# Performance work log

Hardware: AMD Instinct MI355X
Metric: run time of the kernel (lower is better)

## Reference

```python
import jax, jax.numpy as jnp
import numpy as np

EPS = 1e-5
GROUPS = 32
N_HEADS = 8
HEAD_DIM = 64


def setup_inputs() -> dict:
    key = jax.random.key(0)
    ks = jax.random.split(key, 8)
    b, c, d, w, hs = 2, 512, 16, 16, 16
    ctx_len, ctx_dim = 1024, 768
    inner = N_HEADS * HEAD_DIM  # 512
    return {
        "x": jax.random.normal(ks[0], (b, c, d, w, hs), jnp.float32),
        "context": jax.random.normal(ks[1], (b, ctx_len, ctx_dim), jnp.float32),
        "gamma": jnp.ones((c,), jnp.float32),
        "beta": jnp.zeros((c,), jnp.float32),
        "Wq": jax.random.normal(ks[2], (c, inner), jnp.float32) * (c ** -0.5),
        "Wk": jax.random.normal(ks[3], (ctx_dim, inner), jnp.float32) * (ctx_dim ** -0.5),
        "Wv": jax.random.normal(ks[4], (ctx_dim, inner), jnp.float32) * (ctx_dim ** -0.5),
        "Wo": jax.random.normal(ks[5], (inner, c), jnp.float32) * (inner ** -0.5),
        "bo": jnp.zeros((c,), jnp.float32),
    }


def reference(x, context, gamma, beta, Wq, Wk, Wv, Wo, bo):
    b, c, d, w, hs = x.shape
    n = d * w * hs  # sequence length of voxel tokens
    scale = HEAD_DIM ** -0.5

    # GroupNorm over (channels-in-group, spatial)
    xg = x.reshape(b, GROUPS, -1)
    mu = jnp.mean(xg, axis=-1, keepdims=True)
    var = jnp.mean(jnp.square(xg - mu), axis=-1, keepdims=True)
    xn = (xg - mu) * jax.lax.rsqrt(var + EPS)
    xn = xn.reshape(b, c, n) * gamma[None, :, None] + beta[None, :, None]

    x_seq = jnp.swapaxes(x.reshape(b, c, n), 1, 2)   # [b, n, c] residual
    xn_seq = jnp.swapaxes(xn, 1, 2)                   # [b, n, c]

    q = (xn_seq @ Wq).reshape(b, n, N_HEADS, HEAD_DIM)
    k = (context @ Wk).reshape(b, -1, N_HEADS, HEAD_DIM)
    v = (context @ Wv).reshape(b, -1, N_HEADS, HEAD_DIM)

    attn = jax.nn.softmax(jnp.einsum('bqhd,bkhd->bhqk', q, k) * scale, axis=-1)
    out = jnp.einsum('bhqk,bkhd->bqhd', attn, v).reshape(b, n, N_HEADS * HEAD_DIM)

    out = out @ Wo + bo  # dropout is identity in eval mode
    out = out + x_seq
    return jnp.swapaxes(out, 1, 2).reshape(b, c, d, w, hs)
```

## Files before the change

### kernel.cpp

```cpp
#include <hip/hip_runtime.h>
#include <hip/hip_bf16.h>

#define B 2
#define C 512
#define NTOK 4096
#define GROUPS 32
#define CPG 16
#define CTX 1024
#define CDIM 768
#define NH 8
#define HD 64
#define INNER 512
#define EPS 1e-5f
#define KVBLK 64
#define NCH (CTX / KVBLK)
#define LOG2E 1.44269504f

typedef unsigned short bf16_t;
typedef __attribute__((ext_vector_type(8))) short bf16x8;
typedef __attribute__((ext_vector_type(4))) float f32x4;

__device__ __forceinline__ bf16_t f2b(float f) {
    unsigned u = __float_as_uint(f);
    u += 0x7fffu + ((u >> 16) & 1u);
    return (bf16_t)(u >> 16);
}

__device__ __forceinline__ float4 pack8(const float* v) {
    union { ushort s[8]; float4 f; } u;
    #pragma unroll
    for (int j = 0; j < 8; ++j) u.s[j] = f2b(v[j]);
    return u.f;
}

__device__ __forceinline__ unsigned cvtpk(float lo, float hi) {
    unsigned r;
    asm("v_cvt_pk_bf16_f32 %0, %1, %2" : "=v"(r) : "v"(lo), "v"(hi));
    return r;
}

__device__ __forceinline__ int swz(int row, int col) {
    return row * 64 + (col ^ ((row & 7) << 3));
}

__global__ __launch_bounds__(256) void gn_partial_kernel(const float* __restrict__ x,
                                                         float2* __restrict__ partials) {
    int blk = blockIdx.x;
    const float* base = x + (size_t)blk * 4096;
    float s = 0.f, ss = 0.f;
    #pragma unroll
    for (int i = 0; i < 4; ++i) {
        float4 v = *(const float4*)&base[(threadIdx.x + i * 256) * 4];
        s += v.x + v.y + v.z + v.w;
        ss += v.x * v.x + v.y * v.y + v.z * v.z + v.w * v.w;
    }
    #pragma unroll
    for (int o = 32; o > 0; o >>= 1) { s += __shfl_xor(s, o); ss += __shfl_xor(ss, o); }
    __shared__ float ls[2][4];
    int wv = threadIdx.x >> 6, ln = threadIdx.x & 63;
    if (ln == 0) { ls[0][wv] = s; ls[1][wv] = ss; }
    __syncthreads();
    if (threadIdx.x == 0) {
        partials[blk] = make_float2(ls[0][0] + ls[0][1] + ls[0][2] + ls[0][3],
                                    ls[1][0] + ls[1][1] + ls[1][2] + ls[1][3]);
    }
}

__global__ __launch_bounds__(256) void gn_apply_kernel(const float* __restrict__ x,
                                                       const float2* __restrict__ partials,
                                                       const float* __restrict__ gamma,
                                                       const float* __restrict__ beta,
                                                       bf16_t* __restrict__ xn) {
    __shared__ float tile[32][33];
    __shared__ float gmu[2], grs[2];
    int b = blockIdx.z;
    int c0 = blockIdx.y * 32;
    int t0 = blockIdx.x * 32;
    int tid = threadIdx.x;
    if (tid < 32) {
        int gi = tid >> 4, pi = tid & 15;
        float2 pp = partials[b * C + c0 + gi * 16 + pi];
        float s = pp.x, ss = pp.y;
        #pragma unroll
        for (int o = 8; o > 0; o >>= 1) { s += __shfl_xor(s, o); ss += __shfl_xor(ss, o); }
        if (pi == 0) {
            float mu = s / (float)(CPG * NTOK);
            float var = ss / (float)(CPG * NTOK) - mu * mu;
            gmu[gi] = mu;
            grs[gi] = rsqrtf(var + EPS);
        }
    }
    int tt = tid & 31, cr = tid >> 5;
    __syncthreads();
    #pragma unroll
    for (int i = 0; i < 4; ++i) {
        int co = cr + 8 * i;
        int c = c0 + co;
        float mu = gmu[co >> 4], rs = grs[co >> 4];
        float v = x[((size_t)(b * C + c)) * NTOK + t0 + tt];
        tile[co][tt] = (v - mu) * rs * gamma[c] + beta[c];
    }
    __syncthreads();
    #pragma unroll
    for (int i = 0; i < 4; ++i) {
        int t = t0 + cr + 8 * i;
        int c = c0 + tt;
        xn[((size_t)b * NTOK + t) * C + c] = f2b(tile[tt][cr + 8 * i]);
    }
}

__global__ __launch_bounds__(256) void wcast_all_kernel(
    const float* __restrict__ Wq, const float* __restrict__ Wk,
    const float* __restrict__ Wv, const float* __restrict__ Wo,
    bf16_t* __restrict__ Wqt, bf16_t* __restrict__ Wkvt, bf16_t* __restrict__ Wot) {
    int z = blockIdx.z;
    const float* in; bf16_t* out; int K;
    if (z == 0)      { in = Wq; out = Wqt;  K = C; }
    else if (z == 1) { in = Wk; out = Wkvt; K = CDIM; }
    else if (z == 2) { in = Wv; out = Wkvt + (size_t)INNER * CDIM; K = CDIM; }
    else             { in = Wo; out = Wot;  K = INNER; }
    int k0 = blockIdx.x * 32, n0 = blockIdx.y * 32;
    if (k0 >= K) return;
    __shared__ float t[32][33];
    int xx = threadIdx.x & 31, yy = threadIdx.x >> 5;
    #pragma unroll
    for (int i = 0; i < 4; ++i)
        t[yy + 8 * i][xx] = in[(size_t)(k0 + yy + 8 * i) * INNER + n0 + xx];
    __syncthreads();
    #pragma unroll
    for (int i = 0; i < 4; ++i)
        out[(size_t)(n0 + yy + 8 * i) * K + k0 + xx] = f2b(t[xx][yy + 8 * i]);
}

template <int AFP32>
__global__ __launch_bounds__(256) void gemm_qkv_kernel(
    const void* __restrict__ Av, const bf16_t* __restrict__ Bt,
    bf16_t* __restrict__ outK, bf16_t* __restrict__ outV,
    int K, int seqshift, float oscale, int vtrans) {
    __shared__ __align__(16) bf16_t As[64][40];
    __shared__ __align__(16) bf16_t Bs[64][40];
    const int tid = threadIdx.x;
    const int l = tid & 63, w = tid >> 6;
    const int wr = w >> 1, wc = w & 1;
    const int lg = l >> 4, lr = l & 15;
    const int m0 = blockIdx.x * 64, n0 = blockIdx.y * 64;
    const int rowS = tid >> 2, c8 = (tid & 3) * 8;
    const bf16_t* pa16 = AFP32 ? nullptr : (const bf16_t*)Av + (size_t)(m0 + rowS) * K + c8;
    const float*  pa32 = AFP32 ? (const float*)Av + (size_t)(m0 + rowS) * K + c8 : nullptr;
    const bf16_t* pb = Bt + (size_t)(n0 + rowS) * K + c8;
    f32x4 acc[2][2] = {};
    float av[8];
    float4 ra, rb;
    if (AFP32) {
        *(float4*)&av[0] = *(const float4*)pa32;
        *(float4*)&av[4] = *(const float4*)(pa32 + 4);
        ra = pack8(av);
    } else {
        ra = *(const float4*)pa16;
    }
    rb = *(const float4*)pb;
    *(float4*)&As[rowS][c8] = ra;
    *(float4*)&Bs[rowS][c8] = rb;
    for (int k0 = 0; k0 < K; k0 += 32) {
        __syncthreads();
        if (k0 + 32 < K) {
            if (AFP32) {
                *(float4*)&av[0] = *(const float4*)(pa32 + k0 + 32);
                *(float4*)&av[4] = *(const float4*)(pa32 + k0 + 36);
                ra = pack8(av);
            } else {
                ra = *(const float4*)(pa16 + k0 + 32);
            }
            rb = *(const float4*)(pb + k0 + 32);
        }
        bf16x8 af[2], bfm[2];
        af[0]  = *(bf16x8*)&As[wr * 32 + lr][lg * 8];
        af[1]  = *(bf16x8*)&As[wr * 32 + 16 + lr][lg * 8];
        bfm[0] = *(bf16x8*)&Bs[wc * 32 + lr][lg * 8];
        bfm[1] = *(bf16x8*)&Bs[wc * 32 + 16 + lr][lg * 8];
        #pragma unroll
        for (int mi = 0; mi < 2; ++mi)
            #pragma unroll
            for (int ni = 0; ni < 2; ++ni)
                acc[mi][ni] = __builtin_amdgcn_mfma_f32_16x16x32_bf16(af[mi], bfm[ni], acc[mi][ni], 0, 0, 0);
        __syncthreads();
        if (k0 + 32 < K) {
            *(float4*)&As[rowS][c8] = ra;
            *(float4*)&Bs[rowS][c8] = rb;
        }
    }
    const int seqmask = (1 << seqshift) - 1;
    #pragma unroll
    for (int ni = 0; ni < 2; ++ni) {
        int n = n0 + wc * 32 + ni * 16 + lr;
        int nn = n & (INNER - 1);
        int h = nn >> 6, dd = nn & 63;
        bool isV = (n >= INNER);
        #pragma unroll
        for (int mi = 0; mi < 2; ++mi) {
            int mb = m0 + wr * 32 + mi * 16 + lg * 4;
            int bidx = mb >> seqshift, seqb = mb & seqmask;
            if (isV && vtrans) {
                ushort4 pv;
                pv.x = f2b(acc[mi][ni][0] * oscale);
                pv.y = f2b(acc[mi][ni][1] * oscale);
                pv.z = f2b(acc[mi][ni][2] * oscale);
                pv.w = f2b(acc[mi][ni][3] * oscale);
                *(ushort4*)&outV[((size_t)(bidx * NH + h) * HD + dd) * (size_t)(seqmask + 1) + seqb] = pv;
            } else {
                bf16_t* dst = isV ? outV : outK;
                #pragma unroll
                for (int r = 0; r < 4; ++r)
                    dst[(((size_t)(bidx * NH + h) << seqshift) + seqb + r) * HD + dd] =
                        f2b(acc[mi][ni][r] * oscale);
            }
        }
    }
}

__global__ __launch_bounds__(256) void gemm_o_kernel(
    const bf16_t* __restrict__ A, const bf16_t* __restrict__ Bt,
    const float* __restrict__ bo, const float* __restrict__ x,
    float* __restrict__ out) {
    __shared__ __align__(16) bf16_t As[64][40];
    __shared__ __align__(16) bf16_t Bs[64][40];
    const int tid = threadIdx.x;
    const int l = tid & 63, w = tid >> 6;
    const int wr = w >> 1, wc = w & 1;
    const int lg = l >> 4, lr = l & 15;
    const int m0 = blockIdx.x * 64, n0 = blockIdx.y * 64;
    const int rowS = tid >> 2, c8 = (tid & 3) * 8;
    const bf16_t* pa = A  + (size_t)(m0 + rowS) * INNER + c8;
    const bf16_t* pb = Bt + (size_t)(n0 + rowS) * INNER + c8;
    f32x4 acc[2][2] = {};
    float4 ra = *(const float4*)pa;
    float4 rb = *(const float4*)pb;
    *(float4*)&As[rowS][c8] = ra;
    *(float4*)&Bs[rowS][c8] = rb;
    for (int k0 = 0; k0 < INNER; k0 += 32) {
        __syncthreads();
        if (k0 + 32 < INNER) {
            ra = *(const float4*)(pa + k0 + 32);
            rb = *(const float4*)(pb + k0 + 32);
        }
        bf16x8 af[2], bfm[2];
        af[0]  = *(bf16x8*)&As[wr * 32 + lr][lg * 8];
        af[1]  = *(bf16x8*)&As[wr * 32 + 16 + lr][lg * 8];
        bfm[0] = *(bf16x8*)&Bs[wc * 32 + lr][lg * 8];
        bfm[1] = *(bf16x8*)&Bs[wc * 32 + 16 + lr][lg * 8];
        #pragma unroll
        for (int mi = 0; mi < 2; ++mi)
            #pragma unroll
            for (int ni = 0; ni < 2; ++ni)
                acc[mi][ni] = __builtin_amdgcn_mfma_f32_16x16x32_bf16(af[mi], bfm[ni], acc[mi][ni], 0, 0, 0);
        __syncthreads();
        if (k0 + 32 < INNER) {
            *(float4*)&As[rowS][c8] = ra;
            *(float4*)&Bs[rowS][c8] = rb;
        }
    }
    #pragma unroll
    for (int mi = 0; mi < 2; ++mi) {
        int mb = m0 + wr * 32 + mi * 16 + lg * 4;
        int t = mb & (NTOK - 1);
        int bb = mb >> 12;
        #pragma unroll
        for (int ni = 0; ni < 2; ++ni) {
            int cc = n0 + wc * 32 + ni * 16 + lr;
            size_t o = (((size_t)(bb * C + cc)) << 12) + t;
            float4 xr = *(const float4*)&x[o];
            float bias = bo[cc];
            float4 ov;
            ov.x = acc[mi][ni][0] + bias + xr.x;
            ov.y = acc[mi][ni][1] + bias + xr.y;
            ov.z = acc[mi][ni][2] + bias + xr.z;
            ov.w = acc[mi][ni][3] + bias + xr.w;
            *(float4*)&out[o] = ov;
        }
    }
}

__global__ __launch_bounds__(256) void attn_kernel(
    const bf16_t* __restrict__ Q, const bf16_t* __restrict__ Kb,
    const bf16_t* __restrict__ Vt, bf16_t* __restrict__ AO) {
    __shared__ __align__(16) bf16_t Ks[64 * 64];
    __shared__ __align__(16) bf16_t Vs[64 * 64];
    __shared__ __align__(16) bf16_t Ps[4][16 * 64];
    const int tid = threadIdx.x;
    const int l = tid & 63, w = tid >> 6;
    const int lg = l >> 4, lr = l & 15;
    const int bh = blockIdx.x >> 6;
    const int tile = blockIdx.x & 63;
    const int b = bh >> 3, h = bh & 7;
    const int t0 = tile * 64 + w * 16;

    const bf16_t* qbase = Q + ((size_t)bh * NTOK + t0 + lr) * HD;
    bf16x8 qf[2];
    qf[0] = *(const bf16x8*)&qbase[lg * 8];
    qf[1] = *(const bf16x8*)&qbase[32 + lg * 8];

    f32x4 acc[4] = {};
    float mrow = -1e30f;
    float lrow = 0.f;

    const bf16_t* kbase = Kb + (size_t)bh * CTX * HD;
    const bf16_t* vbase = Vt + (size_t)bh * HD * CTX;
    const int srow = tid >> 3, sc8 = (tid & 7) * 8;

    float4 kr0 = *(const float4*)&kbase[(size_t)srow * HD + sc8];
    float4 kr1 = *(const float4*)&kbase[(size_t)(srow + 32) * HD + sc8];
    float4 vr0 = *(const float4*)&vbase[(size_t)srow * CTX + sc8];
    float4 vr1 = *(const float4*)&vbase[(size_t)(srow + 32) * CTX + sc8];
    *(float4*)&Ks[swz(srow, sc8)] = kr0;
    *(float4*)&Ks[swz(srow + 32, sc8)] = kr1;
    *(float4*)&Vs[swz(srow, sc8)] = vr0;
    *(float4*)&Vs[swz(srow + 32, sc8)] = vr1;

    for (int c = 0; c < NCH; ++c) {
        __syncthreads();
        if (c + 1 < NCH) {
            int k1 = (c + 1) * KVBLK;
            kr0 = *(const float4*)&kbase[(size_t)(k1 + srow) * HD + sc8];
            kr1 = *(const float4*)&kbase[(size_t)(k1 + srow + 32) * HD + sc8];
            vr0 = *(const float4*)&vbase[(size_t)srow * CTX + k1 + sc8];
            vr1 = *(const float4*)&vbase[(size_t)(srow + 32) * CTX + k1 + sc8];
        }
        f32x4 sf[4] = {};
        #pragma unroll
        for (int ks = 0; ks < 2; ++ks)
            #pragma unroll
            for (int ni = 0; ni < 4; ++ni) {
                bf16x8 kf = *(bf16x8*)&Ks[swz(ni * 16 + lr, ks * 32 + lg * 8)];
                sf[ni] = __builtin_amdgcn_mfma_f32_16x16x32_bf16(kf, qf[ks], sf[ni], 0, 0, 0);
            }
        float cm = sf[0][0];
        #pragma unroll
        for (int ni = 0; ni < 4; ++ni)
            #pragma unroll
            for (int r = 0; r < 4; ++r) cm = fmaxf(cm, sf[ni][r]);
        cm = fmaxf(cm, __shfl_xor(cm, 16));
        cm = fmaxf(cm, __shfl_xor(cm, 32));
        float mn = fmaxf(mrow, cm);
        float scl = __builtin_amdgcn_exp2f(mrow - mn);
        mrow = mn;
        float p[4][4];
        float rs = 0.f;
        #pragma unroll
        for (int ni = 0; ni < 4; ++ni)
            #pragma unroll
            for (int r = 0; r < 4; ++r) {
                p[ni][r] = __builtin_amdgcn_exp2f(sf[ni][r] - mn);
                rs += p[ni][r];
            }
        rs += __shfl_xor(rs, 16);
        rs += __shfl_xor(rs, 32);
        lrow = lrow * scl + rs;
        #pragma unroll
        for (int ni = 0; ni < 4; ++ni) {
            unsigned pk0 = cvtpk(p[ni][0], p[ni][1]);
            unsigned pk1 = cvtpk(p[ni][2], p[ni][3]);
            *(uint2*)&Ps[w][swz(lr, ni * 16 + 4 * lg)] = make_uint2(pk0, pk1);
        }
        float sclr[4];
        #pragma unroll
        for (int r = 0; r < 4; ++r)
            sclr[r] = __shfl(scl, (l & 48) | (4 * lg + r));
        #pragma unroll
        for (int ni = 0; ni < 4; ++ni)
            #pragma unroll
            for (int r = 0; r < 4; ++r) acc[ni][r] *= sclr[r];
        #pragma unroll
        for (int ks = 0; ks < 2; ++ks) {
            bf16x8 pf = *(bf16x8*)&Ps[w][swz(lr, ks * 32 + 8 * lg)];
            #pragma unroll
            for (int ni = 0; ni < 4; ++ni) {
                bf16x8 vf = *(bf16x8*)&Vs[swz(ni * 16 + lr, ks * 32 + lg * 8)];
                acc[ni] = __builtin_amdgcn_mfma_f32_16x16x32_bf16(pf, vf, acc[ni], 0, 0, 0);
            }
        }
        __syncthreads();
        if (c + 1 < NCH) {
            *(float4*)&Ks[swz(srow, sc8)] = kr0;
            *(float4*)&Ks[swz(srow + 32, sc8)] = kr1;
            *(float4*)&Vs[swz(srow, sc8)] = vr0;
            *(float4*)&Vs[swz(srow + 32, sc8)] = vr1;
        }
    }

    float lfin[4];
    #pragma unroll
    for (int r = 0; r < 4; ++r)
        lfin[r] = __shfl(lrow, (l & 48) | (4 * lg + r));
    #pragma unroll
    for (int ni = 0; ni < 4; ++ni)
        #pragma unroll
        for (int r = 0; r < 4; ++r) {
            int t = t0 + lg * 4 + r;
            AO[((size_t)b * NTOK + t) * INNER + h * HD + ni * 16 + lr] =
                f2b(acc[ni][r] / lfin[r]);
        }
}

extern "C" void kernel_launch(void* const* d_in, const int* in_sizes, int n_in,
                              void* d_out, int out_size, void* d_ws, size_t ws_size,
                              hipStream_t stream) {
    const float* x       = (const float*)d_in[0];
    const float* context = (const float*)d_in[1];
    const float* gamma   = (const float*)d_in[2];
    const float* beta    = (const float*)d_in[3];
    const float* Wq      = (const float*)d_in[4];
    const float* Wk      = (const float*)d_in[5];
    const float* Wv      = (const float*)d_in[6];
    const float* Wo      = (const float*)d_in[7];
    const float* bo      = (const float*)d_in[8];
    float* out = (float*)d_out;

    char* p = (char*)d_ws;
    float2* parts = (float2*)p;          p += 1024 * sizeof(float2);
    bf16_t* xn   = (bf16_t*)p;           p += (size_t)B * NTOK * C * 2;
    bf16_t* Wqt  = (bf16_t*)p;           p += (size_t)INNER * C * 2;
    bf16_t* Wkvt = (bf16_t*)p;           p += (size_t)2 * INNER * CDIM * 2;
    bf16_t* Wot  = (bf16_t*)p;           p += (size_t)C * INNER * 2;
    bf16_t* qb   = (bf16_t*)p;           p += (size_t)B * NH * NTOK * HD * 2;
    bf16_t* kb   = (bf16_t*)p;           p += (size_t)B * NH * CTX * HD * 2;
    bf16_t* vb   = (bf16_t*)p;           p += (size_t)B * NH * CTX * HD * 2;
    bf16_t* ao   = (bf16_t*)p;           p += (size_t)B * NTOK * INNER * 2;

    hipLaunchKernelGGL(gn_partial_kernel, dim3(B * C), dim3(256), 0, stream, x, parts);
    hipLaunchKernelGGL(gn_apply_kernel, dim3(NTOK / 32, C / 32, B), dim3(256), 0, stream,
                       x, parts, gamma, beta, xn);
    hipLaunchKernelGGL(wcast_all_kernel, dim3(24, 16, 4), dim3(256), 0, stream,
                       Wq, Wk, Wv, Wo, Wqt, Wkvt, Wot);
    hipLaunchKernelGGL((gemm_qkv_kernel<0>), dim3(128, 8), dim3(256), 0, stream,
                       (const void*)xn, Wqt, qb, qb, C, 12, 0.125f * LOG2E, 0);
    hipLaunchKernelGGL((gemm_qkv_kernel<1>), dim3(32, 16), dim3(256), 0, stream,
                       (const void*)context, Wkvt, kb, vb, CDIM, 10, 1.0f, 1);
    hipLaunchKernelGGL(attn_kernel, dim3(B * NH * (NTOK / 64)), dim3(256), 0, stream,
                       qb, kb, vb, ao);
    hipLaunchKernelGGL(gemm_o_kernel, dim3(128, 8), dim3(256), 0, stream,
                       ao, Wot, bo, x, out);
}
```

Before: 171.5 us.

## Merge GN stats and weight cast kernels; use 64-deep K steps in GEMMs

Fuses the GroupNorm partial-sum kernel and the weight transpose/cast kernel into a single launch, removing one kernel launch. Both GEMM kernels now stage two 32-wide K slices per iteration, halving the number of barrier pairs per K loop and issuing twice as many global loads ahead of the MFMAs, at the cost of more LDS and registers. The attention epilogue replaces per-element division with a hardware reciprocal multiply, which slightly changes rounding.

```diff
diff --git a/kernel.cpp b/kernel.cpp
--- a/kernel.cpp
+++ b/kernel.cpp
@@ -43,27 +43,51 @@
     return row * 64 + (col ^ ((row & 7) << 3));
 }
 
-__global__ __launch_bounds__(256) void gn_partial_kernel(const float* __restrict__ x,
-                                                         float2* __restrict__ partials) {
+__global__ __launch_bounds__(256) void prep_kernel(
+    const float* __restrict__ x, float2* __restrict__ partials,
+    const float* __restrict__ Wq, const float* __restrict__ Wk,
+    const float* __restrict__ Wv, const float* __restrict__ Wo,
+    bf16_t* __restrict__ Wqt, bf16_t* __restrict__ Wkvt, bf16_t* __restrict__ Wot) {
     int blk = blockIdx.x;
-    const float* base = x + (size_t)blk * 4096;
-    float s = 0.f, ss = 0.f;
-    #pragma unroll
-    for (int i = 0; i < 4; ++i) {
-        float4 v = *(const float4*)&base[(threadIdx.x + i * 256) * 4];
-        s += v.x + v.y + v.z + v.w;
-        ss += v.x * v.x + v.y * v.y + v.z * v.z + v.w * v.w;
-    }
-    #pragma unroll
-    for (int o = 32; o > 0; o >>= 1) { s += __shfl_xor(s, o); ss += __shfl_xor(ss, o); }
-    __shared__ float ls[2][4];
-    int wv = threadIdx.x >> 6, ln = threadIdx.x & 63;
-    if (ln == 0) { ls[0][wv] = s; ls[1][wv] = ss; }
+    if (blk < B * C) {
+        const float* base = x + (size_t)blk * 4096;
+        float s = 0.f, ss = 0.f;
+        #pragma unroll
+        for (int i = 0; i < 4; ++i) {
+            float4 v = *(const float4*)&base[(threadIdx.x + i * 256) * 4];
+            s += v.x + v.y + v.z + v.w;
+            ss += v.x * v.x + v.y * v.y + v.z * v.z + v.w * v.w;
+        }
+        #pragma unroll
+        for (int o = 32; o > 0; o >>= 1) { s += __shfl_xor(s, o); ss += __shfl_xor(ss, o); }
+        __shared__ float ls[2][4];
+        int wv = threadIdx.x >> 6, ln = threadIdx.x & 63;
+        if (ln == 0) { ls[0][wv] = s; ls[1][wv] = ss; }
+        __syncthreads();
+        if (threadIdx.x == 0)
+            partials[blk] = make_float2(ls[0][0] + ls[0][1] + ls[0][2] + ls[0][3],
+                                        ls[1][0] + ls[1][1] + ls[1][2] + ls[1][3]);
+        return;
+    }
+    int id = blk - B * C;
+    int z = id / 384;
+    int rem = id - z * 384;
+    int k0 = (rem % 24) * 32, n0 = (rem / 24) * 32;
+    const float* in; bf16_t* out; int K;
+    if (z == 0)      { in = Wq; out = Wqt;  K = C; }
+    else if (z == 1) { in = Wk; out = Wkvt; K = CDIM; }
+    else if (z == 2) { in = Wv; out = Wkvt + (size_t)INNER * CDIM; K = CDIM; }
+    else             { in = Wo; out = Wot;  K = INNER; }
+    if (k0 >= K) return;
+    __shared__ float t[32][33];
+    int xx = threadIdx.x & 31, yy = threadIdx.x >> 5;
+    #pragma unroll
+    for (int i = 0; i < 4; ++i)
+        t[yy + 8 * i][xx] = in[(size_t)(k0 + yy + 8 * i) * INNER + n0 + xx];
     __syncthreads();
-    if (threadIdx.x == 0) {
-        partials[blk] = make_float2(ls[0][0] + ls[0][1] + ls[0][2] + ls[0][3],
-                                    ls[1][0] + ls[1][1] + ls[1][2] + ls[1][3]);
-    }
+    #pragma unroll
+    for (int i = 0; i < 4; ++i)
+        out[(size_t)(n0 + yy + 8 * i) * K + k0 + xx] = f2b(t[xx][yy + 8 * i]);
 }
 
 __global__ __launch_bounds__(256) void gn_apply_kernel(const float* __restrict__ x,
@@ -109,36 +133,13 @@
     }
 }
 
-__global__ __launch_bounds__(256) void wcast_all_kernel(
-    const float* __restrict__ Wq, const float* __restrict__ Wk,
-    const float* __restrict__ Wv, const float* __restrict__ Wo,
-    bf16_t* __restrict__ Wqt, bf16_t* __restrict__ Wkvt, bf16_t* __restrict__ Wot) {
-    int z = blockIdx.z;
-    const float* in; bf16_t* out; int K;
-    if (z == 0)      { in = Wq; out = Wqt;  K = C; }
-    else if (z == 1) { in = Wk; out = Wkvt; K = CDIM; }
-    else if (z == 2) { in = Wv; out = Wkvt + (size_t)INNER * CDIM; K = CDIM; }
-    else             { in = Wo; out = Wot;  K = INNER; }
-    int k0 = blockIdx.x * 32, n0 = blockIdx.y * 32;
-    if (k0 >= K) return;
-    __shared__ float t[32][33];
-    int xx = threadIdx.x & 31, yy = threadIdx.x >> 5;
-    #pragma unroll
-    for (int i = 0; i < 4; ++i)
-        t[yy + 8 * i][xx] = in[(size_t)(k0 + yy + 8 * i) * INNER + n0 + xx];
-    __syncthreads();
-    #pragma unroll
-    for (int i = 0; i < 4; ++i)
-        out[(size_t)(n0 + yy + 8 * i) * K + k0 + xx] = f2b(t[xx][yy + 8 * i]);
-}
-
 template <int AFP32>
 __global__ __launch_bounds__(256) void gemm_qkv_kernel(
     const void* __restrict__ Av, const bf16_t* __restrict__ Bt,
     bf16_t* __restrict__ outK, bf16_t* __restrict__ outV,
     int K, int seqshift, float oscale, int vtrans) {
-    __shared__ __align__(16) bf16_t As[64][40];
-    __shared__ __align__(16) bf16_t Bs[64][40];
+    __shared__ __align__(16) bf16_t As[2][64][40];
+    __shared__ __align__(16) bf16_t Bs[2][64][40];
     const int tid = threadIdx.x;
     const int l = tid & 63, w = tid >> 6;
     const int wr = w >> 1, wc = w & 1;
@@ -150,45 +151,56 @@
     const bf16_t* pb = Bt + (size_t)(n0 + rowS) * K + c8;
     f32x4 acc[2][2] = {};
     float av[8];
-    float4 ra, rb;
-    if (AFP32) {
-        *(float4*)&av[0] = *(const float4*)pa32;
-        *(float4*)&av[4] = *(const float4*)(pa32 + 4);
-        ra = pack8(av);
-    } else {
-        ra = *(const float4*)pa16;
-    }
-    rb = *(const float4*)pb;
-    *(float4*)&As[rowS][c8] = ra;
-    *(float4*)&Bs[rowS][c8] = rb;
-    for (int k0 = 0; k0 < K; k0 += 32) {
-        __syncthreads();
-        if (k0 + 32 < K) {
-            if (AFP32) {
-                *(float4*)&av[0] = *(const float4*)(pa32 + k0 + 32);
-                *(float4*)&av[4] = *(const float4*)(pa32 + k0 + 36);
-                ra = pack8(av);
-            } else {
-                ra = *(const float4*)(pa16 + k0 + 32);
-            }
-            rb = *(const float4*)(pb + k0 + 32);
-        }
-        bf16x8 af[2], bfm[2];
-        af[0]  = *(bf16x8*)&As[wr * 32 + lr][lg * 8];
-        af[1]  = *(bf16x8*)&As[wr * 32 + 16 + lr][lg * 8];
-        bfm[0] = *(bf16x8*)&Bs[wc * 32 + lr][lg * 8];
-        bfm[1] = *(bf16x8*)&Bs[wc * 32 + 16 + lr][lg * 8];
-        #pragma unroll
-        for (int mi = 0; mi < 2; ++mi)
-            #pragma unroll
-            for (int ni = 0; ni < 2; ++ni)
-                acc[mi][ni] = __builtin_amdgcn_mfma_f32_16x16x32_bf16(af[mi], bfm[ni], acc[mi][ni], 0, 0, 0);
-        __syncthreads();
-        if (k0 + 32 < K) {
-            *(float4*)&As[rowS][c8] = ra;
-            *(float4*)&Bs[rowS][c8] = rb;
-        }
-    }
+    float4 ra0, ra1, rb0, rb1;
+    #define LOADA(dst, off) do { \
+        if (AFP32) { \
+            *(float4*)&av[0] = *(const float4*)(pa32 + (off)); \
+            *(float4*)&av[4] = *(const float4*)(pa32 + (off) + 4); \
+            dst = pack8(av); \
+        } else { dst = *(const float4*)(pa16 + (off)); } } while (0)
+    LOADA(ra0, 0);
+    LOADA(ra1, 32);
+    rb0 = *(const float4*)pb;
+    rb1 = *(const float4*)(pb + 32);
+    *(float4*)&As[0][rowS][c8] = ra0;
+    *(float4*)&As[1][rowS][c8] = ra1;
+    *(float4*)&Bs[0][rowS][c8] = rb0;
+    *(float4*)&Bs[1][rowS][c8] = rb1;
+    const int NIT = K >> 6;
+    for (int it = 0; it < NIT; ++it) {
+        __syncthreads();
+        if (it + 1 < NIT) {
+            int k1 = (it + 1) << 6;
+            LOADA(ra0, k1);
+            LOADA(ra1, k1 + 32);
+            rb0 = *(const float4*)(pb + k1);
+            rb1 = *(const float4*)(pb + k1 + 32);
+        }
+        bf16x8 af[2][2], bfm[2][2];
+        #pragma unroll
+        for (int ks = 0; ks < 2; ++ks) {
+            af[0][ks]  = *(bf16x8*)&As[ks][wr * 32 + lr][lg * 8];
+            af[1][ks]  = *(bf16x8*)&As[ks][wr * 32 + 16 + lr][lg * 8];
+            bfm[0][ks] = *(bf16x8*)&Bs[ks][wc * 32 + lr][lg * 8];
+            bfm[1][ks] = *(bf16x8*)&Bs[ks][wc * 32 + 16 + lr][lg * 8];
+        }
+        #pragma unroll
+        for (int ks = 0; ks < 2; ++ks)
+            #pragma unroll
+            for (int mi = 0; mi < 2; ++mi)
+                #pragma unroll
+                for (int ni = 0; ni < 2; ++ni)
+                    acc[mi][ni] = __builtin_amdgcn_mfma_f32_16x16x32_bf16(
+                        af[mi][ks], bfm[ni][ks], acc[mi][ni], 0, 0, 0);
+        __syncthreads();
+        if (it + 1 < NIT) {
+            *(float4*)&As[0][rowS][c8] = ra0;
+            *(float4*)&As[1][rowS][c8] = ra1;
+            *(float4*)&Bs[0][rowS][c8] = rb0;
+            *(float4*)&Bs[1][rowS][c8] = rb1;
+        }
+    }
+    #undef LOADA
     const int seqmask = (1 << seqshift) - 1;
     #pragma unroll
     for (int ni = 0; ni < 2; ++ni) {
@@ -222,8 +234,8 @@
     const bf16_t* __restrict__ A, const bf16_t* __restrict__ Bt,
     const float* __restrict__ bo, const float* __restrict__ x,
     float* __restrict__ out) {
-    __shared__ __align__(16) bf16_t As[64][40];
-    __shared__ __align__(16) bf16_t Bs[64][40];
+    __shared__ __align__(16) bf16_t As[2][64][40];
+    __shared__ __align__(16) bf16_t Bs[2][64][40];
     const int tid = threadIdx.x;
     const int l = tid & 63, w = tid >> 6;
     const int wr = w >> 1, wc = w & 1;
@@ -233,30 +245,46 @@
     const bf16_t* pa = A  + (size_t)(m0 + rowS) * INNER + c8;
     const bf16_t* pb = Bt + (size_t)(n0 + rowS) * INNER + c8;
     f32x4 acc[2][2] = {};
-    float4 ra = *(const float4*)pa;
-    float4 rb = *(const float4*)pb;
-    *(float4*)&As[rowS][c8] = ra;
-    *(float4*)&Bs[rowS][c8] = rb;
-    for (int k0 = 0; k0 < INNER; k0 += 32) {
-        __syncthreads();
-        if (k0 + 32 < INNER) {
-            ra = *(const float4*)(pa + k0 + 32);
-            rb = *(const float4*)(pb + k0 + 32);
-        }
-        bf16x8 af[2], bfm[2];
-        af[0]  = *(bf16x8*)&As[wr * 32 + lr][lg * 8];
-        af[1]  = *(bf16x8*)&As[wr * 32 + 16 + lr][lg * 8];
-        bfm[0] = *(bf16x8*)&Bs[wc * 32 + lr][lg * 8];
-        bfm[1] = *(bf16x8*)&Bs[wc * 32 + 16 + lr][lg * 8];
-        #pragma unroll
-        for (int mi = 0; mi < 2; ++mi)
-            #pragma unroll
-            for (int ni = 0; ni < 2; ++ni)
-                acc[mi][ni] = __builtin_amdgcn_mfma_f32_16x16x32_bf16(af[mi], bfm[ni], acc[mi][ni], 0, 0, 0);
-        __syncthreads();
-        if (k0 + 32 < INNER) {
-            *(float4*)&As[rowS][c8] = ra;
-            *(float4*)&Bs[rowS][c8] = rb;
+    float4 ra0 = *(const float4*)pa;
+    float4 ra1 = *(const float4*)(pa + 32);
+    float4 rb0 = *(const float4*)pb;
+    float4 rb1 = *(const float4*)(pb + 32);
+    *(float4*)&As[0][rowS][c8] = ra0;
+    *(float4*)&As[1][rowS][c8] = ra1;
+    *(float4*)&Bs[0][rowS][c8] = rb0;
+    *(float4*)&Bs[1][rowS][c8] = rb1;
+    const int NIT = INNER >> 6;
+    for (int it = 0; it < NIT; ++it) {
+        __syncthreads();
+        if (it + 1 < NIT) {
+            int k1 = (it + 1) << 6;
+            ra0 = *(const float4*)(pa + k1);
+            ra1 = *(const float4*)(pa + k1 + 32);
+            rb0 = *(const float4*)(pb + k1);
+            rb1 = *(const float4*)(pb + k1 + 32);
+        }
+        bf16x8 af[2][2], bfm[2][2];
+        #pragma unroll
+        for (int ks = 0; ks < 2; ++ks) {
+            af[0][ks]  = *(bf16x8*)&As[ks][wr * 32 + lr][lg * 8];
+            af[1][ks]  = *(bf16x8*)&As[ks][wr * 32 + 16 + lr][lg * 8];
+            bfm[0][ks] = *(bf16x8*)&Bs[ks][wc * 32 + lr][lg * 8];
+            bfm[1][ks] = *(bf16x8*)&Bs[ks][wc * 32 + 16 + lr][lg * 8];
+        }
+        #pragma unroll
+        for (int ks = 0; ks < 2; ++ks)
+            #pragma unroll
+            for (int mi = 0; mi < 2; ++mi)
+                #pragma unroll
+                for (int ni = 0; ni < 2; ++ni)
+                    acc[mi][ni] = __builtin_amdgcn_mfma_f32_16x16x32_bf16(
+                        af[mi][ks], bfm[ni][ks], acc[mi][ni], 0, 0, 0);
+        __syncthreads();
+        if (it + 1 < NIT) {
+            *(float4*)&As[0][rowS][c8] = ra0;
+            *(float4*)&As[1][rowS][c8] = ra1;
+            *(float4*)&Bs[0][rowS][c8] = rb0;
+            *(float4*)&Bs[1][rowS][c8] = rb1;
         }
     }
     #pragma unroll
@@ -387,17 +415,17 @@
         }
     }
 
-    float lfin[4];
+    float linv[4];
     #pragma unroll
     for (int r = 0; r < 4; ++r)
-        lfin[r] = __shfl(lrow, (l & 48) | (4 * lg + r));
+        linv[r] = __builtin_amdgcn_rcpf(__shfl(lrow, (l & 48) | (4 * lg + r)));
     #pragma unroll
     for (int ni = 0; ni < 4; ++ni)
         #pragma unroll
         for (int r = 0; r < 4; ++r) {
             int t = t0 + lg * 4 + r;
             AO[((size_t)b * NTOK + t) * INNER + h * HD + ni * 16 + lr] =
-                f2b(acc[ni][r] / lfin[r]);
+                f2b(acc[ni][r] * linv[r]);
         }
 }
 
@@ -426,11 +454,10 @@
     bf16_t* vb   = (bf16_t*)p;           p += (size_t)B * NH * CTX * HD * 2;
     bf16_t* ao   = (bf16_t*)p;           p += (size_t)B * NTOK * INNER * 2;
 
-    hipLaunchKernelGGL(gn_partial_kernel, dim3(B * C), dim3(256), 0, stream, x, parts);
+    hipLaunchKernelGGL(prep_kernel, dim3(B * C + 1536), dim3(256), 0, stream,
+                       x, parts, Wq, Wk, Wv, Wo, Wqt, Wkvt, Wot);
     hipLaunchKernelGGL(gn_apply_kernel, dim3(NTOK / 32, C / 32, B), dim3(256), 0, stream,
                        x, parts, gamma, beta, xn);
-    hipLaunchKernelGGL(wcast_all_kernel, dim3(24, 16, 4), dim3(256), 0, stream,
-                       Wq, Wk, Wv, Wo, Wqt, Wkvt, Wot);
     hipLaunchKernelGGL((gemm_qkv_kernel<0>), dim3(128, 8), dim3(256), 0, stream,
                        (const void*)xn, Wqt, qb, qb, C, 12, 0.125f * LOG2E, 0);
     hipLaunchKernelGGL((gemm_qkv_kernel<1>), dim3(32, 16), dim3(256), 0, stream,
```

New measurement: 163.3 us. 4.8% less time.
